# Kernel optimization log

Measured on AMD Instinct MI355X. Metric: run time of the kernel, lower is better.

The kernel has to match this reference:

```python
import jax, jax.numpy as jnp
import numpy as np

_SAMPLING_EPS = 1e-5
B, V = 256, 128000


def _apply_min_p(logits, min_p):
    # probs >= min_p * max_prob  <=>  keep; else logit -> -inf
    probs = jax.nn.softmax(logits, axis=-1)
    max_probs = jnp.max(probs, axis=-1, keepdims=True)
    keep = probs >= (min_p[:, None] * max_probs)
    return jnp.where(keep, logits, -jnp.inf)


def _apply_top_k_top_p(logits, top_k, top_p):
    # Sort ascending once; derive per-row keep-thresholds for both filters.
    logits_sort = jnp.sort(logits, axis=-1)  # [B, V] ascending
    # top-k threshold: value at position V-k (kth largest)
    k_idx = jnp.clip(V - top_k, 0, V - 1).astype(jnp.int32)
    k_thresh = jnp.take_along_axis(logits_sort, k_idx[:, None], axis=-1)  # [B,1]
    # top-p: on ascending-sorted probs, token is kept iff cumsum > 1 - p
    probs_sort = jax.nn.softmax(logits_sort, axis=-1)
    probs_cum = jnp.cumsum(probs_sort, axis=-1)
    kept = probs_cum > (1.0 - top_p[:, None])
    kept = kept.at[:, -1].set(True)  # always keep the max-prob token
    p_thresh = jnp.min(jnp.where(kept, logits_sort, jnp.inf), axis=-1, keepdims=True)
    thresh = jnp.maximum(k_thresh, p_thresh)
    return jnp.where(logits >= thresh, logits, -jnp.inf)


def setup_inputs() -> dict:
    key = jax.random.key(0)
    k1, k2, k3, k4, k5 = jax.random.split(key, 5)
    logits = jax.random.normal(k1, (B, V), jnp.float32)
    temperature = jax.random.uniform(k2, (B,), jnp.float32, 0.1, 1.5)
    temperature = temperature.at[:8].set(0.0)  # greedy rows
    min_p = jax.random.uniform(k3, (B,), jnp.float32, 0.0, 0.2)
    top_k = jax.random.randint(k4, (B,), 1, 64).astype(jnp.int32)
    top_p = jax.random.uniform(k5, (B,), jnp.float32, 0.5, 1.0)
    return {"logits": logits, "temperature": temperature, "min_p": min_p,
            "top_k": top_k, "top_p": top_p}


def reference(logits, temperature, min_p, top_k, top_p):
    logits = logits.astype(jnp.float32)
    greedy = jnp.argmax(logits, axis=-1)  # [B]
    # safe temperature divide (greedy rows have temp ~ 0 but are overridden)
    safe_t = jnp.where(temperature < _SAMPLING_EPS, 1.0, temperature)
    scaled = logits / safe_t[:, None]
    scaled = _apply_min_p(scaled, min_p)
    masked = _apply_top_k_top_p(scaled, top_k, top_p)
    # Gumbel-max trick == categorical sampling from softmax(masked)
    u = jax.random.uniform(jax.random.key(42), masked.shape, jnp.float32, 1e-10, 1.0)
    gumbel = -jnp.log(-jnp.log(u))
    random_sampled = jnp.argmax(masked + gumbel, axis=-1)
    sampled = jnp.where(temperature < _SAMPLING_EPS, greedy, random_sampled)
    return sampled[:, None]  # sampled_token_ids [B, 1]
```

## Files before the change

kernel.cpp:

```cpp
#include <hip/hip_runtime.h>
#include <hip/hip_cooperative_groups.h>
#include <stdint.h>

namespace cg = cooperative_groups;

typedef unsigned long long u64;
typedef unsigned int u32;

#define VOCAB 128000
#define NV4   32000
#define HV4   16000
#define NROWS 256
#define BLK   1024
#define NW    16
#define NB    4096
#define CAPL  2048
#define CAPLS 4096
#define SEPS  1e-5f
#define LN2X40 27.725887222397812f

#define WS_MASSH   0ull
#define WS_LIST    16777216ull
#define WS_CNTH    20971520ull
#define WS_PARTS   29360128ull
#define WS_PARTK   29362176ull
#define WS_PARTGV  29364224ull
#define WS_PARTGI  29366272ull
#define WS_LL      29368320ull
#define WS_KP      29369344ull
#define WS_NEED    29370368ull

__device__ __forceinline__ u32 f2key(float f){
  u32 u = __float_as_uint(f);
  return (u & 0x80000000u) ? ~u : (u | 0x80000000u);
}
__device__ __forceinline__ float key2f(u32 k){
  u32 u = (k & 0x80000000u) ? (k ^ 0x80000000u) : ~k;
  return __uint_as_float(u);
}

__device__ __forceinline__ void tf2x32(u32 x0, u32 x1, u32 &o0, u32 &o1){
  const u32 k0 = 0u, k1 = 42u, k2 = 0u ^ 42u ^ 0x1BD11BDAu;
  x0 += k0; x1 += k1;
#define TFR(r) { x0 += x1; x1 = (x1 << (r)) | (x1 >> (32 - (r))); x1 ^= x0; }
  TFR(13) TFR(15) TFR(26) TFR(6)
  x0 += k1; x1 += k2 + 1u;
  TFR(17) TFR(29) TFR(16) TFR(24)
  x0 += k2; x1 += k0 + 2u;
  TFR(13) TFR(15) TFR(26) TFR(6)
  x0 += k0; x1 += k1 + 3u;
  TFR(17) TFR(29) TFR(16) TFR(24)
  x0 += k1; x1 += k2 + 4u;
  TFR(13) TFR(15) TFR(26) TFR(6)
  x0 += k2; x1 += k0 + 5u;
#undef TFR
  o0 = x0; o1 = x1;
}
__device__ __forceinline__ u32 gumbel_bits(u32 i){
  u32 o0, o1; tf2x32(0u, i, o0, o1);
  return o0 ^ o1;
}
__device__ __forceinline__ float bits2gumbel(u32 b){
  float f = __uint_as_float(0x3F800000u | (b >> 9)) - 1.0f;
  float u = fmaxf(1e-10f, f + 1e-10f);
  return -logf(-logf(u));
}

__device__ __forceinline__ void cross4096_u32(
    const u32* arr, u32* aux, u32 target, u32* out_idx, u32* out_before, int t)
{
  aux[t] = arr[4*t+0] + arr[4*t+1] + arr[4*t+2] + arr[4*t+3];
  __syncthreads();
  if (t < 64){
    u32 gs = 0u;
    #pragma unroll
    for (int j=0;j<16;j++) gs += aux[t*16+j];
    u32 pref = gs;
    #pragma unroll
    for (int d=1; d<64; d<<=1){ u32 v = __shfl_up(pref, d, 64); if (t >= d) pref += v; }
    u64 bal = __ballot(pref > target);
    int g = bal ? (__ffsll((long long)bal) - 1) : 63;
    u32 pg = __shfl(pref, g, 64);
    u32 gg = __shfl(gs, g, 64);
    if (t == 0){
      u32 c = pg - gg;
      u32 idx = (u32)(g*64 + 63);
      for (int j=0;j<16;j++){
        u32 v = aux[g*16+j];
        if (c + v > target){
          int base = (g*16+j)*4;
          for (int q=0;q<4;q++){
            u32 w = arr[base+q];
            if (c + w > target){ idx = (u32)(base+q); goto doneu; }
            c += w;
          }
        }
        c += v;
      }
      doneu:
      *out_idx = idx; *out_before = c;
    }
  }
}

__device__ __forceinline__ void cross4096_u64(
    const u64* arr, u64* aux, u64 target, u32* out_idx, u64* out_before, int t)
{
  aux[t] = arr[4*t+0] + arr[4*t+1] + arr[4*t+2] + arr[4*t+3];
  __syncthreads();
  if (t < 64){
    u64 gs = 0ull;
    #pragma unroll
    for (int j=0;j<16;j++) gs += aux[t*16+j];
    u64 pref = gs;
    #pragma unroll
    for (int d=1; d<64; d<<=1){
      u64 v = __shfl_up((unsigned long long)pref, d, 64); if (t >= d) pref += v;
    }
    u64 bal = __ballot(pref > target);
    int g = bal ? (__ffsll((long long)bal) - 1) : 63;
    u64 pg = __shfl((unsigned long long)pref, g, 64);
    u64 gg = __shfl((unsigned long long)gs, g, 64);
    if (t == 0){
      u64 c = pg - gg;
      u32 idx = (u32)(g*64 + 63);
      for (int j=0;j<16;j++){
        u64 v = aux[g*16+j];
        if (c + v > target){
          int base = (g*16+j)*4;
          for (int q=0;q<4;q++){
            u64 w = arr[base+q];
            if (c + w > target){ idx = (u32)(base+q); goto donev; }
            c += w;
          }
        }
        c += v;
      }
      donev:
      *out_idx = idx; *out_before = c;
    }
  }
}

__device__ __forceinline__ void cross4096_mass(
    const u64* arr, u64* aux, float topp_v, u64* out_target,
    u32* out_idx, u64* out_before, int t)
{
  aux[t] = arr[4*t+0] + arr[4*t+1] + arr[4*t+2] + arr[4*t+3];
  __syncthreads();
  if (t < 64){
    u64 gs = 0ull;
    #pragma unroll
    for (int j=0;j<16;j++) gs += aux[t*16+j];
    u64 pref = gs;
    #pragma unroll
    for (int d=1; d<64; d<<=1){
      u64 v = __shfl_up((unsigned long long)pref, d, 64); if (t >= d) pref += v;
    }
    u64 total = __shfl((unsigned long long)pref, 63, 64);
    u64 target = (u64)((double)(1.0f - topp_v) * (double)total);
    u64 bal = __ballot(pref > target);
    int g = bal ? (__ffsll((long long)bal) - 1) : 63;
    u64 pg = __shfl((unsigned long long)pref, g, 64);
    u64 gg = __shfl((unsigned long long)gs, g, 64);
    if (t == 0){
      u64 c = pg - gg;
      u32 idx = (u32)(g*64 + 63);
      for (int j=0;j<16;j++){
        u64 v = aux[g*16+j];
        if (c + v > target){
          int base = (g*16+j)*4;
          for (int q=0;q<4;q++){
            u64 w = arr[base+q];
            if (c + w > target){ idx = (u32)(base+q); goto donem; }
            c += w;
          }
        }
        c += v;
      }
      donem:
      *out_target = target; *out_idx = idx; *out_before = c;
    }
  }
}

__device__ __forceinline__ void cross256_u32(const u32* arr, u32 target, u32* out_idx, int t){
  if (t < 64){
    u32 gs = arr[4*t+0]+arr[4*t+1]+arr[4*t+2]+arr[4*t+3];
    u32 pref = gs;
    #pragma unroll
    for (int d=1; d<64; d<<=1){ u32 v=__shfl_up(pref,d,64); if (t>=d) pref+=v; }
    u64 bal = __ballot(pref > target);
    int g = bal ? (__ffsll((long long)bal)-1) : 63;
    u32 pg=__shfl(pref,g,64), gg=__shfl(gs,g,64);
    if (t==0){
      u32 c = pg-gg; u32 idx=(u32)(g*4+3);
      for (int q=0;q<4;q++){ u32 w=arr[g*4+q]; if (c+w>target){ idx=(u32)(g*4+q); break; } c+=w; }
      *out_idx = idx;
    }
  }
}
__device__ __forceinline__ void cross256_u64(const u64* arr, u64 target, u32* out_idx, int t){
  if (t < 64){
    u64 gs = arr[4*t+0]+arr[4*t+1]+arr[4*t+2]+arr[4*t+3];
    u64 pref = gs;
    #pragma unroll
    for (int d=1; d<64; d<<=1){
      u64 v=__shfl_up((unsigned long long)pref,d,64); if (t>=d) pref+=v;
    }
    u64 bal = __ballot(pref > target);
    int g = bal ? (__ffsll((long long)bal)-1) : 63;
    u64 pg=__shfl((unsigned long long)pref,g,64), gg=__shfl((unsigned long long)gs,g,64);
    if (t==0){
      u64 c = pg-gg; u32 idx=(u32)(g*4+3);
      for (int q=0;q<4;q++){ u64 w=arr[g*4+q]; if (c+w>target){ idx=(u32)(g*4+q); break; } c+=w; }
      *out_idx = idx;
    }
  }
}

__device__ __forceinline__ void msmerge(float &m1, float &S1, float m2, float S2){
  float mm = fmaxf(m1, m2);
  if (mm == -INFINITY){ m1 = mm; S1 = 0.0f; return; }
  S1 = S1*__expf(m1-mm) + S2*__expf(m2-mm);
  m1 = mm;
}

__device__ __forceinline__ void argmax_write(
    float best, u32 bi, float* wrf, u32* wru, int ln, int wv, int b, int* out)
{
  #pragma unroll
  for (int d=32; d>0; d>>=1){
    float c2=__shfl_down(best,d,64); u32 i2=__shfl_down(bi,d,64);
    if (c2>best || (c2==best && i2<bi)){best=c2;bi=i2;}
  }
  if (ln==0){ wrf[wv]=best; wru[wv]=bi; }
  __syncthreads();
  if (wv==0){
    float b1=(ln<NW)?wrf[ln]:-INFINITY; u32 i1=(ln<NW)?wru[ln]:0xFFFFFFFFu;
    #pragma unroll
    for (int d=32; d>0; d>>=1){
      float b2=__shfl_down(b1,d,64); u32 i2=__shfl_down(i1,d,64);
      if (b2>b1 || (b2==b1 && i2<i1)){b1=b2;i1=i2;}
    }
    if (ln==0) out[b]=(int)i1;
  }
}

__global__ __launch_bounds__(BLK, 8) void k_coop(
    const float* __restrict__ logits, const float* __restrict__ temp,
    const float* __restrict__ minp, const int* __restrict__ topk,
    const float* __restrict__ topp, int* __restrict__ out, char* __restrict__ ws)
{
  cg::grid_group grid = cg::this_grid();

  __shared__ u32 cnt[NB];
  __shared__ u64 massI[NB];
  __shared__ u64 list[CAPL];
  __shared__ u64 aux64[BLK];
  __shared__ float wrf1[NW];
  __shared__ u32  wru1[NW], wru2[NW];
  __shared__ u32 sh_idx, sh_bef32, sh_lstar, sh_u1, sh_u2;
  __shared__ u64 sh_bef64, sh_tfix;

  u32* aux32 = (u32*)aux64;
  u64* massH  = (u64*)(ws + WS_MASSH);
  u64* wsList = (u64*)(ws + WS_LIST);
  u32* cntH   = (u32*)(ws + WS_CNTH);
  float* partS  = (float*)(ws + WS_PARTS);
  u32*   partK  = (u32*)(ws + WS_PARTK);
  float* partGV = (float*)(ws + WS_PARTGV);
  u32*   partGI = (u32*)(ws + WS_PARTGI);
  u32*   LL     = (u32*)(ws + WS_LL);
  u32*   KP     = (u32*)(ws + WS_KP);

  const int bid = blockIdx.x;
  const int r = bid >> 1;
  const int h = bid & 1;
  const int t = threadIdx.x;
  const int ln = t & 63, wv = t >> 6;
  const float T = temp[r];
  const bool greedy = (T < SEPS);
  const float invT = greedy ? 1.0f : (1.0f / T);
  const float* row = logits + (size_t)r * VOCAB;
  const float4* row4 = (const float4*)row;
  const int hb4 = h * HV4, he4 = hb4 + HV4;

  if (t == 0 && h == 0){ LL[r] = 0u; KP[r] = 0u; }
  if (greedy){
    float M = -INFINITY; u32 Mi = 0xFFFFFFFFu;
    for (int i = hb4 + t; i < he4; i += BLK){
      float4 q = row4[i];
      #pragma unroll
      for (int j=0;j<4;j++){
        float l = (&q.x)[j]; u32 gi = (u32)(i*4+j);
        if (l > M){ M = l; Mi = gi; }
      }
    }
    #pragma unroll
    for (int d=32; d>0; d>>=1){
      float M2=__shfl_down(M,d,64); u32 I2=__shfl_down(Mi,d,64);
      if (M2>M || (M2==M && I2<Mi)){ M=M2; Mi=I2; }
    }
    if (ln==0){ wrf1[wv]=M; wru1[wv]=Mi; }
    __syncthreads();
    if (t==0){
      float b1=wrf1[0]; u32 i1=wru1[0];
      for (int w=1; w<NW; w++){
        if (wrf1[w]>b1 || (wrf1[w]==b1 && wru1[w]<i1)){ b1=wrf1[w]; i1=wru1[w]; }
      }
      partGV[bid]=b1; partGI[bid]=i1;
    }
  } else {
    for (int i=t;i<NB;i+=BLK) cnt[i]=0u;
    __syncthreads();
    u32 km = 0u;
    float S0=0.0f,S1=0.0f,S2=0.0f,S3=0.0f;
#define PA(LV, SS) { \
    float l_=(LV); u32 k_=f2key(l_); \
    if (k_>km) km=k_; \
    atomicAdd(&cnt[k_>>20], 1u); \
    SS += __expf(l_*invT); }
    for (int i = hb4 + t; i < he4; i += 2*BLK){
      float4 qa = row4[i];
      int i2 = i + BLK; bool h2 = (i2 < he4);
      float4 qb; if (h2) qb = row4[i2];
      PA(qa.x,S0) PA(qa.y,S1) PA(qa.z,S2) PA(qa.w,S3)
      if (h2){ PA(qb.x,S0) PA(qb.y,S1) PA(qb.z,S2) PA(qb.w,S3) }
    }
#undef PA
    float S = (S0+S1)+(S2+S3);
    #pragma unroll
    for (int d=32; d>0; d>>=1){
      S += __shfl_down(S,d,64);
      u32 k2 = __shfl_down(km,d,64); if (k2>km) km=k2;
    }
    if (ln==0){ wrf1[wv]=S; wru1[wv]=km; }
    __syncthreads();
    for (int i=t;i<NB;i+=BLK) cntH[(size_t)bid*NB + i] = cnt[i];
    if (t==0){
      float St=0.0f; u32 kt=0u;
      for (int w=0; w<NW; w++){ St += wrf1[w]; if (wru1[w]>kt) kt=wru1[w]; }
      partS[bid]=St; partK[bid]=kt;
    }
  }
  __threadfence();
  grid.sync();

  float m=0.0f, Z=1.0f, cs=0.0f;
  u32 b1k=0u, r1=1u, lstar=0u, CLB=0u;
  int tk=1; bool kcert=false, fastOK=false;

  if (greedy){
    if (h==0 && t==0){
      float vA=partGV[bid], vB=partGV[bid+1];
      u32 iA=partGI[bid], iB=partGI[bid+1];
      out[r] = (vB>vA || (vB==vA && iB<iA)) ? (int)iB : (int)iA;
    }
  } else {
    const int pb = bid ^ 1;
    for (int i=t;i<NB;i+=BLK) cnt[i] += cntH[(size_t)pb*NB + i];
    {
      u32 kA = partK[bid & ~1], kB = partK[bid | 1];
      float SA = partS[bid & ~1], SB = partS[bid | 1];
      u32 kmax = kA > kB ? kA : kB;
      m = key2f(kmax) * invT;
      Z = (SA + SB) * __expf(-m);
    }
    cs = LN2X40 - m;
    __syncthreads();

    tk = topk[r]; if (tk < 1) tk = 1; if (tk > VOCAB) tk = VOCAB;
    cross4096_u32(cnt, aux32, (u32)(VOCAB - tk), &sh_idx, &sh_bef32, t);
    __syncthreads();
    b1k = sh_idx;
    r1  = (u32)(VOCAB - tk + 1) - sh_bef32;

    if (wv==0){
      const float rhs = minp[r] * (1.0f / Z);
      u32 lo = 0u, hi = 0xFF800000u;
      while (hi - lo > 64u){
        u32 step = (hi - lo) >> 6;
        u32 k = lo + (u32)(ln + 1) * step;
        float e = __expf(fmaf(key2f(k), invT, -m));
        u64 bal = __ballot((e / Z) >= rhs);
        if (bal){
          u32 g = (u32)(__ffsll((long long)bal) - 1);
          hi = lo + (g + 1u) * step;
          lo = lo + g * step;
        } else {
          lo += 64u * step;
        }
      }
      u32 k = lo + 1u + (u32)ln;
      bool ok = (k <= hi);
      float e = __expf(fmaf(key2f(k), invT, -m));
      u64 bal = __ballot(ok && ((e / Z) >= rhs));
      if (ln==0) sh_lstar = bal ? (lo + 1u + (u32)(__ffsll((long long)bal) - 1)) : hi;
    }
    __syncthreads();
    lstar = sh_lstar;
    const u32 bl = lstar >> 20;

    {
      u32 pa=0u, pc=0u;
      for (int i=t;i<NB;i+=BLK){
        u32 c = cnt[i];
        if ((u32)i > bl)   pa += c;
        if ((u32)i >= b1k) pc += c;
      }
      #pragma unroll
      for (int d=32; d>0; d>>=1){ pa += __shfl_down(pa,d,64); pc += __shfl_down(pc,d,64); }
      if (ln==0){ wru1[wv]=pa; wru2[wv]=pc; }
      __syncthreads();
      if (t==0){
        u32 a=0u, c2=0u;
        for (int w=0; w<NW; w++){ a += wru1[w]; c2 += wru2[w]; }
        sh_u1 = a; sh_u2 = c2;
      }
      __syncthreads();
    }
    const u32 Kmin = sh_u1;
    kcert = (Kmin >= (u32)tk);
    CLB = kcert ? b1k : bl;
    const u32 listCnt = kcert ? sh_u2 : (Kmin + cnt[bl]);
    fastOK = (listCnt <= (u32)CAPL);
  }

  if (!greedy){
    for (int i=t;i<NB;i+=BLK) massI[i]=0ull;
    __syncthreads();
    u32 kc = 0u;
#define PC(LV, IDX) { \
    float l_ = (LV); u32 key_ = f2key(l_); \
    if (key_ >= lstar){ \
      kc++; \
      u64 lm_ = (u64)__expf(fmaf(l_, invT, cs)); \
      if (lm_) atomicAdd(&massI[key_>>20], lm_); \
    } \
    bool cand_ = fastOK && ((key_>>20) >= CLB); \
    u64 bal_ = __ballot(cand_); \
    if (cand_){ \
      u32 lead_ = (u32)__ffsll((long long)bal_) - 1u; \
      u32 base_ = 0u; \
      if ((u32)ln == lead_) base_ = atomicAdd(&LL[r], (u32)__popcll(bal_)); \
      base_ = __shfl(base_, (int)lead_, 64); \
      u32 p_ = base_ + (u32)__popcll(bal_ & ((1ull << ln) - 1ull)); \
      if (p_ < CAPL) wsList[(size_t)r*CAPL + p_] = ((u64)key_ << 32) | (u64)(u32)(IDX); \
    } }
    for (int i = hb4 + t; i < he4; i += 2*BLK){
      float4 qa = row4[i];
      int i2 = i + BLK; bool h2 = (i2 < he4);
      float4 qb; if (h2) qb = row4[i2];
      PC(qa.x,i*4+0) PC(qa.y,i*4+1) PC(qa.z,i*4+2) PC(qa.w,i*4+3)
      if (h2){ PC(qb.x,i2*4+0) PC(qb.y,i2*4+1) PC(qb.z,i2*4+2) PC(qb.w,i2*4+3) }
    }
#undef PC
    #pragma unroll
    for (int d=32; d>0; d>>=1) kc += __shfl_down(kc, d, 64);
    if (ln==0) wru1[wv] = kc;
    __syncthreads();
    if (t==0){
      u32 K2=0u; for (int w=0;w<NW;w++) K2 += wru1[w];
      atomicAdd(&KP[r], K2);
    }
    if (h==1){
      for (int i=t;i<NB;i+=BLK) massH[(size_t)bid*NB + i] = massI[i];
    }
  }
  __threadfence();
  grid.sync();

  if (greedy || h != 0) return;

  for (int i=t;i<NB;i+=BLK) massI[i] += massH[(size_t)(bid+1)*NB + i];
  __syncthreads();
  const u32 K = KP[r];
  const bool kval = (K >= (u32)tk);
  u32 llen = LL[r]; if (llen > (u32)CAPL) llen = CAPL;

  cross4096_mass(massI, aux64, topp[r], &sh_tfix, &sh_idx, &sh_bef64, t);
  __syncthreads();
  const u32 b1p = sh_idx;
  const u64 t1  = sh_tfix - sh_bef64;
  const bool needK = kval && (b1p <= b1k);
  const bool needP = (!kval) || (b1p >= b1k);

  u32 kkey = 0u, pkey = 0u;

  if (fastOK){
    for (u32 i=t; i<llen; i+=BLK) list[i] = wsList[(size_t)r*CAPL + i];
    __syncthreads();
    if (needK){
      for (int i=t;i<NB;i+=BLK) cnt[i]=0u;
      __syncthreads();
      for (u32 i=t; i<llen; i+=BLK){
        u32 key = (u32)(list[i]>>32);
        if ((key>>20) == b1k) atomicAdd(&cnt[(key>>8)&0xFFFu], 1u);
      }
      __syncthreads();
      cross4096_u32(cnt, aux32, r1-1u, &sh_idx, &sh_bef32, t);
      __syncthreads();
      u32 b2k = sh_idx, r2 = r1 - sh_bef32;
      u32 prefk = (b1k<<12) | b2k;
      for (int i=t;i<256;i+=BLK) cnt[i]=0u;
      __syncthreads();
      for (u32 i=t; i<llen; i+=BLK){
        u32 key = (u32)(list[i]>>32);
        if ((key>>8) == prefk) atomicAdd(&cnt[key&0xFFu], 1u);
      }
      __syncthreads();
      cross256_u32(cnt, r2-1u, &sh_idx, t);
      __syncthreads();
      kkey = (prefk<<8) | sh_idx;
    }
    if (needP){
      for (int i=t;i<NB;i+=BLK) massI[i]=0ull;
      __syncthreads();
      for (u32 i=t; i<llen; i+=BLK){
        u32 key = (u32)(list[i]>>32);
        if ((key>>20) == b1p && key >= lstar){
          u64 lm = (u64)__expf(fmaf(key2f(key), invT, cs));
          if (lm) atomicAdd(&massI[(key>>8)&0xFFFu], lm);
        }
      }
      __syncthreads();
      cross4096_u64(massI, aux64, t1, &sh_idx, &sh_bef64, t);
      __syncthreads();
      u32 b2p = sh_idx; u64 t2 = t1 - sh_bef64;
      u32 prefp = (b1p<<12) | b2p;
      for (int i=t;i<256;i+=BLK) massI[i]=0ull;
      __syncthreads();
      for (u32 i=t; i<llen; i+=BLK){
        u32 key = (u32)(list[i]>>32);
        if ((key>>8) == prefp && key >= lstar){
          u64 lm = (u64)__expf(fmaf(key2f(key), invT, cs));
          if (lm) atomicAdd(&massI[key&0xFFu], lm);
        }
      }
      __syncthreads();
      cross256_u64(massI, t2, &sh_idx, t);
      __syncthreads();
      pkey = (prefp<<8) | sh_idx;
    }
    const u32 thrkey = kkey > pkey ? kkey : pkey;

    float best = -INFINITY; u32 bi = 0xFFFFFFFFu;
    for (u32 i=t; i<llen; i+=BLK){
      u64 e = list[i];
      u32 key = (u32)(e>>32);
      if (key >= thrkey){
        u32 idx = (u32)e;
        u32 c = (u32)r * (u32)VOCAB + idx;
        float cand = key2f(key)*invT + bits2gumbel(gumbel_bits(c));
        if (cand > best || (cand == best && idx < bi)){ best = cand; bi = idx; }
      }
    }
    argmax_write(best, bi, wrf1, wru1, ln, wv, r, out);
    return;
  }

  for (int i=t;i<NB;i+=BLK) cnt[i]=0u;
  { __syncthreads(); }
  for (int i=t;i<NB;i+=BLK) massI[i]=0ull;
  __syncthreads();
  for (int i=t; i<NV4; i+=BLK){
    float4 q = row4[i];
    #pragma unroll
    for (int j=0;j<4;j++){
      float l = (&q.x)[j]; u32 key = f2key(l); u32 hb = key>>20;
      if (needK && hb == b1k) atomicAdd(&cnt[(key>>8)&0xFFFu], 1u);
      if (needP && hb == b1p && key >= lstar){
        u64 lm = (u64)__expf(fmaf(l, invT, cs));
        if (lm) atomicAdd(&massI[(key>>8)&0xFFFu], lm);
      }
    }
  }
  __syncthreads();
  u32 b2k = 0u, r2 = 1u, b2p = 0u; u64 t2 = 0ull;
  if (needK){
    cross4096_u32(cnt, aux32, r1-1u, &sh_idx, &sh_bef32, t);
    __syncthreads();
    b2k = sh_idx; r2 = r1 - sh_bef32;
  }
  if (needP){
    cross4096_u64(massI, aux64, t1, &sh_idx, &sh_bef64, t);
    __syncthreads();
    b2p = sh_idx; t2 = t1 - sh_bef64;
  }
  const u32 prefk = (b1k<<12) | b2k;
  const u32 prefp = (b1p<<12) | b2p;
  for (int i=t;i<256;i+=BLK){ cnt[i]=0u; massI[i]=0ull; }
  __syncthreads();
  for (int i=t; i<NV4; i+=BLK){
    float4 q = row4[i];
    #pragma unroll
    for (int j=0;j<4;j++){
      float l = (&q.x)[j]; u32 key = f2key(l);
      if (needK && (key>>8) == prefk) atomicAdd(&cnt[key&0xFFu], 1u);
      if (needP && (key>>8) == prefp && key >= lstar){
        u64 lm = (u64)__expf(fmaf(l, invT, cs));
        if (lm) atomicAdd(&massI[key&0xFFu], lm);
      }
    }
  }
  __syncthreads();
  if (needK){
    cross256_u32(cnt, r2-1u, &sh_idx, t);
    __syncthreads();
    kkey = (prefk<<8) | sh_idx;
  }
  if (needP){
    cross256_u64(massI, t2, &sh_idx, t);
    __syncthreads();
    pkey = (prefp<<8) | sh_idx;
  }
  const float thrf = key2f(kkey > pkey ? kkey : pkey);
  float best = -INFINITY; u32 bi = 0xFFFFFFFFu;
  for (int i=t; i<NV4; i+=BLK){
    float4 q = row4[i];
    #pragma unroll
    for (int j=0;j<4;j++){
      float l = (&q.x)[j];
      if (l >= thrf){
        u32 idx = (u32)(i*4+j);
        u32 c = (u32)r * (u32)VOCAB + idx;
        float cand = l*invT + bits2gumbel(gumbel_bits(c));
        if (cand > best || (cand == best && idx < bi)){ best = cand; bi = idx; }
      }
    }
  }
  argmax_write(best, bi, wrf1, wru1, ln, wv, r, out);
}

__global__ __launch_bounds__(BLK) void k_single(
    const float* __restrict__ logits, const float* __restrict__ temp,
    const float* __restrict__ minp, const int* __restrict__ topk,
    const float* __restrict__ topp, int* __restrict__ out)
{
  __shared__ u32 cnt[NB];
  __shared__ u64 massI[NB];
  __shared__ u64 list[CAPLS];
  __shared__ u64 aux64[BLK];
  __shared__ float wrf1[NW], wrf2[NW];
  __shared__ u32  wru1[NW], wru2[NW];
  __shared__ float sh_m, sh_Z;
  __shared__ u32 sh_lstar, sh_len, sh_idx, sh_bef32, sh_u1, sh_u2, sh_u3;
  __shared__ u64 sh_bef64, sh_tfix;

  u32* aux32 = (u32*)aux64;

  const int b = blockIdx.x;
  const int t = threadIdx.x;
  const int ln = t & 63, wv = t >> 6;
  const float T = temp[b];
  const float* row = logits + (size_t)b * VOCAB;
  const float4* row4 = (const float4*)row;

  if (T < SEPS){
    float M = -INFINITY; u32 Mi = 0xFFFFFFFFu;
    for (int i=t; i<NV4; i+=BLK){
      float4 q = row4[i];
      #pragma unroll
      for (int j=0;j<4;j++){
        float l = (&q.x)[j]; u32 gi = (u32)(i*4+j);
        if (l > M){ M = l; Mi = gi; }
      }
    }
    argmax_write(M, Mi, wrf1, wru1, ln, wv, b, out);
    return;
  }

  const float invT = 1.0f / T;
  for (int i=t;i<NB;i+=BLK){ cnt[i]=0u; massI[i]=0ull; }
  if (t==0) sh_len=0u;
  __syncthreads();

  float ms0=-INFINITY,S0=0.0f, ms1=-INFINITY,S1=0.0f,
        ms2=-INFINITY,S2=0.0f, ms3=-INFINITY,S3=0.0f;
#define ONLINE(LV, MS, SS) { \
    float l_ = (LV); \
    atomicAdd(&cnt[f2key(l_)>>20], 1u); \
    float s_ = l_ * invT; \
    float d_ = s_ - MS; \
    float e_ = __expf(-fabsf(d_)); \
    if (d_ > 0.0f){ SS = fmaf(SS, e_, 1.0f); MS = s_; } else { SS += e_; } \
  }
  for (int i=t; i<NV4; i+=2*BLK){
    float4 qa = row4[i];
    int i2 = i + BLK; bool h2 = (i2 < NV4);
    float4 qb; if (h2) qb = row4[i2];
    ONLINE(qa.x,ms0,S0) ONLINE(qa.y,ms1,S1) ONLINE(qa.z,ms2,S2) ONLINE(qa.w,ms3,S3)
    if (h2){
      ONLINE(qb.x,ms0,S0) ONLINE(qb.y,ms1,S1) ONLINE(qb.z,ms2,S2) ONLINE(qb.w,ms3,S3)
    }
  }
#undef ONLINE
  msmerge(ms0,S0,ms1,S1); msmerge(ms2,S2,ms3,S3); msmerge(ms0,S0,ms2,S2);
  #pragma unroll
  for (int d=32; d>0; d>>=1){
    float mz = __shfl_down(ms0, d, 64); float Sz = __shfl_down(S0, d, 64);
    msmerge(ms0, S0, mz, Sz);
  }
  if (ln==0){ wrf1[wv]=ms0; wrf2[wv]=S0; }
  __syncthreads();
  if (wv==0){
    float m1 = (ln<NW)? wrf1[ln] : -INFINITY;
    float Sx = (ln<NW)? wrf2[ln] : 0.0f;
    #pragma unroll
    for (int d=32; d>0; d>>=1){
      float mz=__shfl_down(m1,d,64); float Sz=__shfl_down(Sx,d,64);
      msmerge(m1, Sx, mz, Sz);
    }
    if (ln==0){ sh_m = m1; sh_Z = Sx; }
  }
  __syncthreads();
  const float m = sh_m, Z = sh_Z;

  int tk = topk[b]; if (tk < 1) tk = 1; if (tk > VOCAB) tk = VOCAB;
  cross4096_u32(cnt, aux32, (u32)(VOCAB - tk), &sh_idx, &sh_bef32, t);
  __syncthreads();
  const u32 b1k = sh_idx;
  const u32 r1  = (u32)(VOCAB - tk + 1) - sh_bef32;

  if (wv==0){
    const float rhs = minp[b] * (1.0f / Z);
    u32 lo = 0u, hi = 0xFF800000u;
    while (hi - lo > 64u){
      u32 step = (hi - lo) >> 6;
      u32 k = lo + (u32)(ln + 1) * step;
      float e = __expf(fmaf(key2f(k), invT, -m));
      u64 bal = __ballot((e / Z) >= rhs);
      if (bal){
        u32 g = (u32)(__ffsll((long long)bal) - 1);
        hi = lo + (g + 1u) * step;
        lo = lo + g * step;
      } else {
        lo += 64u * step;
      }
    }
    u32 k = lo + 1u + (u32)ln;
    bool ok = (k <= hi);
    float e = __expf(fmaf(key2f(k), invT, -m));
    u64 bal = __ballot(ok && ((e / Z) >= rhs));
    if (ln==0) sh_lstar = bal ? (lo + 1u + (u32)(__ffsll((long long)bal) - 1)) : hi;
  }
  __syncthreads();
  const u32 lstar = sh_lstar;
  const u32 bl = lstar >> 20;

  {
    u32 pa=0u, pc=0u;
    for (int i=t;i<NB;i+=BLK){
      u32 c = cnt[i];
      if ((u32)i > bl)   pa += c;
      if ((u32)i >= b1k) pc += c;
    }
    #pragma unroll
    for (int d=32; d>0; d>>=1){ pa += __shfl_down(pa,d,64); pc += __shfl_down(pc,d,64); }
    if (ln==0){ wru1[wv]=pa; wru2[wv]=pc; }
    __syncthreads();
    if (t==0){
      u32 a=0u, c2=0u;
      for (int w=0; w<NW; w++){ a += wru1[w]; c2 += wru2[w]; }
      sh_u1 = a; sh_u2 = c2;
    }
    __syncthreads();
  }
  const u32 Kmin = sh_u1;
  const bool kcert = (Kmin >= (u32)tk);
  const u32 CLB = kcert ? b1k : bl;
  const u32 listlen = kcert ? sh_u2 : (Kmin + cnt[bl]);
  const bool fastOK = (listlen <= (u32)CAPLS);
  const float cs = LN2X40 - m;

  u32 kc = 0u;
#define P2E(LV, IDX) { \
    float l_ = (LV); u32 key_ = f2key(l_); \
    if (key_ >= lstar){ \
      kc++; \
      u64 lm_ = (u64)__expf(fmaf(l_, invT, cs)); \
      if (lm_) atomicAdd(&massI[key_>>20], lm_); \
    } \
    if (fastOK && (key_>>20) >= CLB){ \
      u32 p_ = atomicAdd(&sh_len, 1u); \
      if (p_ < CAPLS) list[p_] = ((u64)key_ << 32) | (u64)(u32)(IDX); \
    } \
  }
  for (int i=t; i<NV4; i+=2*BLK){
    float4 qa = row4[i];
    int i2 = i + BLK; bool h2 = (i2 < NV4);
    float4 qb; if (h2) qb = row4[i2];
    P2E(qa.x, i*4+0) P2E(qa.y, i*4+1) P2E(qa.z, i*4+2) P2E(qa.w, i*4+3)
    if (h2){
      P2E(qb.x, i2*4+0) P2E(qb.y, i2*4+1) P2E(qb.z, i2*4+2) P2E(qb.w, i2*4+3)
    }
  }
#undef P2E
  #pragma unroll
  for (int d=32; d>0; d>>=1) kc += __shfl_down(kc, d, 64);
  if (ln==0) wru1[wv] = kc;
  __syncthreads();
  if (t==0){ u32 K2=0u; for (int w=0;w<NW;w++) K2 += wru1[w]; sh_u3 = K2; }
  __syncthreads();
  const u32 K = sh_u3;
  const bool kval = (K >= (u32)tk);
  const u32 llen = sh_len;

  cross4096_mass(massI, aux64, topp[b], &sh_tfix, &sh_idx, &sh_bef64, t);
  __syncthreads();
  const u32 b1p = sh_idx;
  const u64 t1  = sh_tfix - sh_bef64;
  const bool needK = kval && (b1p <= b1k);
  const bool needP = (!kval) || (b1p >= b1k);

  u32 kkey = 0u, pkey = 0u;

  if (fastOK){
    if (needK){
      for (int i=t;i<NB;i+=BLK) cnt[i]=0u;
      __syncthreads();
      for (u32 i=t; i<llen; i+=BLK){
        u32 key = (u32)(list[i]>>32);
        if ((key>>20) == b1k) atomicAdd(&cnt[(key>>8)&0xFFFu], 1u);
      }
      __syncthreads();
      cross4096_u32(cnt, aux32, r1-1u, &sh_idx, &sh_bef32, t);
      __syncthreads();
      u32 b2k = sh_idx, r2 = r1 - sh_bef32;
      u32 prefk = (b1k<<12) | b2k;
      for (int i=t;i<256;i+=BLK) cnt[i]=0u;
      __syncthreads();
      for (u32 i=t; i<llen; i+=BLK){
        u32 key = (u32)(list[i]>>32);
        if ((key>>8) == prefk) atomicAdd(&cnt[key&0xFFu], 1u);
      }
      __syncthreads();
      cross256_u32(cnt, r2-1u, &sh_idx, t);
      __syncthreads();
      kkey = (prefk<<8) | sh_idx;
    }
    if (needP){
      for (int i=t;i<NB;i+=BLK) massI[i]=0ull;
      __syncthreads();
      for (u32 i=t; i<llen; i+=BLK){
        u32 key = (u32)(list[i]>>32);
        if ((key>>20) == b1p && key >= lstar){
          u64 lm = (u64)__expf(fmaf(key2f(key), invT, cs));
          if (lm) atomicAdd(&massI[(key>>8)&0xFFFu], lm);
        }
      }
      __syncthreads();
      cross4096_u64(massI, aux64, t1, &sh_idx, &sh_bef64, t);
      __syncthreads();
      u32 b2p = sh_idx; u64 t2 = t1 - sh_bef64;
      u32 prefp = (b1p<<12) | b2p;
      for (int i=t;i<256;i+=BLK) massI[i]=0ull;
      __syncthreads();
      for (u32 i=t; i<llen; i+=BLK){
        u32 key = (u32)(list[i]>>32);
        if ((key>>8) == prefp && key >= lstar){
          u64 lm = (u64)__expf(fmaf(key2f(key), invT, cs));
          if (lm) atomicAdd(&massI[key&0xFFu], lm);
        }
      }
      __syncthreads();
      cross256_u64(massI, t2, &sh_idx, t);
      __syncthreads();
      pkey = (prefp<<8) | sh_idx;
    }
    const u32 thrkey = kkey > pkey ? kkey : pkey;

    float best = -INFINITY; u32 bi = 0xFFFFFFFFu;
    for (u32 i=t; i<llen; i+=BLK){
      u64 e = list[i];
      u32 key = (u32)(e>>32);
      if (key >= thrkey){
        u32 idx = (u32)e;
        u32 c = (u32)b * (u32)VOCAB + idx;
        float cand = key2f(key)*invT + bits2gumbel(gumbel_bits(c));
        if (cand > best || (cand == best && idx < bi)){ best = cand; bi = idx; }
      }
    }
    argmax_write(best, bi, wrf1, wru1, ln, wv, b, out);
    return;
  }

  for (int i=t;i<NB;i+=BLK){ cnt[i]=0u; massI[i]=0ull; }
  __syncthreads();
  for (int i=t; i<NV4; i+=BLK){
    float4 q = row4[i];
    #pragma unroll
    for (int j=0;j<4;j++){
      float l = (&q.x)[j]; u32 key = f2key(l); u32 hb = key>>20;
      if (needK && hb == b1k) atomicAdd(&cnt[(key>>8)&0xFFFu], 1u);
      if (needP && hb == b1p && key >= lstar){
        u64 lm = (u64)__expf(fmaf(l, invT, cs));
        if (lm) atomicAdd(&massI[(key>>8)&0xFFFu], lm);
      }
    }
  }
  __syncthreads();
  u32 b2k = 0u, r2 = 1u, b2p = 0u; u64 t2 = 0ull;
  if (needK){
    cross4096_u32(cnt, aux32, r1-1u, &sh_idx, &sh_bef32, t);
    __syncthreads();
    b2k = sh_idx; r2 = r1 - sh_bef32;
  }
  if (needP){
    cross4096_u64(massI, aux64, t1, &sh_idx, &sh_bef64, t);
    __syncthreads();
    b2p = sh_idx; t2 = t1 - sh_bef64;
  }
  const u32 prefk = (b1k<<12) | b2k;
  const u32 prefp = (b1p<<12) | b2p;
  for (int i=t;i<256;i+=BLK){ cnt[i]=0u; massI[i]=0ull; }
  __syncthreads();
  for (int i=t; i<NV4; i+=BLK){
    float4 q = row4[i];
    #pragma unroll
    for (int j=0;j<4;j++){
      float l = (&q.x)[j]; u32 key = f2key(l);
      if (needK && (key>>8) == prefk) atomicAdd(&cnt[key&0xFFu], 1u);
      if (needP && (key>>8) == prefp && key >= lstar){
        u64 lm = (u64)__expf(fmaf(l, invT, cs));
        if (lm) atomicAdd(&massI[key&0xFFu], lm);
      }
    }
  }
  __syncthreads();
  if (needK){
    cross256_u32(cnt, r2-1u, &sh_idx, t);
    __syncthreads();
    kkey = (prefk<<8) | sh_idx;
  }
  if (needP){
    cross256_u64(massI, t2, &sh_idx, t);
    __syncthreads();
    pkey = (prefp<<8) | sh_idx;
  }
  const float thrf = key2f(kkey > pkey ? kkey : pkey);
  float best = -INFINITY; u32 bi = 0xFFFFFFFFu;
  for (int i=t; i<NV4; i+=BLK){
    float4 q = row4[i];
    #pragma unroll
    for (int j=0;j<4;j++){
      float l = (&q.x)[j];
      if (l >= thrf){
        u32 idx = (u32)(i*4+j);
        u32 c = (u32)b * (u32)VOCAB + idx;
        float cand = l*invT + bits2gumbel(gumbel_bits(c));
        if (cand > best || (cand == best && idx < bi)){ best = cand; bi = idx; }
      }
    }
  }
  argmax_write(best, bi, wrf1, wru1, ln, wv, b, out);
}

extern "C" void kernel_launch(void* const* d_in, const int* in_sizes, int n_in,
                              void* d_out, int out_size, void* d_ws, size_t ws_size,
                              hipStream_t stream)
{
  const float* logits = (const float*)d_in[0];
  const float* temp   = (const float*)d_in[1];
  const float* minp   = (const float*)d_in[2];
  const int*   topk   = (const int*)d_in[3];
  const float* topp   = (const float*)d_in[4];
  int* out = (int*)d_out;
  char* ws = (char*)d_ws;

  int maxb = 0;
  hipError_t oe = hipOccupancyMaxActiveBlocksPerMultiprocessor(&maxb, k_coop, BLK, 0);
  const bool coop_ok = (ws_size >= (size_t)WS_NEED) && (oe == hipSuccess) && (maxb >= 2);

  if (coop_ok){
    void* args[] = { (void*)&logits, (void*)&temp, (void*)&minp, (void*)&topk,
                     (void*)&topp, (void*)&out, (void*)&ws };
    hipLaunchCooperativeKernel(k_coop, dim3(2*NROWS), dim3(BLK), args, 0, stream);
  } else {
    hipLaunchKernelGGL(k_single, dim3(NROWS), dim3(BLK), 0, stream,
                       logits, temp, minp, topk, topp, out);
  }
}
```

Baseline: 59.40 us.

## Replace grid-wide syncs with pairwise flag handshakes between row-half blocks

Swaps the two cooperative grid.sync barriers for per-pair flag signalling in global memory, so each block waits only for its partner block handling the other half of the same row. Greedy rows exit early, and the second-half block exits after publishing its mass histogram. This is meant to remove the cost of grid-wide barriers and the stalls caused by the slowest rows. In exchange it adds a memset launch to clear the flags and relies on spin-waits on flags, which assume both blocks of a pair are co-resident.

Measured after the change: 59.21 us. About the same (-0.3%).

```diff
diff --git a/kernel.cpp b/kernel.cpp
--- a/kernel.cpp
+++ b/kernel.cpp
@@ -1,8 +1,5 @@
 #include <hip/hip_runtime.h>
-#include <hip/hip_cooperative_groups.h>
 #include <stdint.h>
-
-namespace cg = cooperative_groups;
 
 typedef unsigned long long u64;
 typedef unsigned int u32;
@@ -28,7 +25,9 @@
 #define WS_PARTGI  29366272ull
 #define WS_LL      29368320ull
 #define WS_KP      29369344ull
-#define WS_NEED    29370368ull
+#define WS_FLAGA   29370368ull
+#define WS_FLAGC   29372416ull
+#define WS_NEED    29374464ull
 
 __device__ __forceinline__ u32 f2key(float f){
   u32 u = __float_as_uint(f);
@@ -252,8 +251,6 @@
     const float* __restrict__ minp, const int* __restrict__ topk,
     const float* __restrict__ topp, int* __restrict__ out, char* __restrict__ ws)
 {
-  cg::grid_group grid = cg::this_grid();
-
   __shared__ u32 cnt[NB];
   __shared__ u64 massI[NB];
   __shared__ u64 list[CAPL];
@@ -273,6 +270,8 @@
   u32*   partGI = (u32*)(ws + WS_PARTGI);
   u32*   LL     = (u32*)(ws + WS_LL);
   u32*   KP     = (u32*)(ws + WS_KP);
+  u32*   flagA  = (u32*)(ws + WS_FLAGA);
+  u32*   flagC  = (u32*)(ws + WS_FLAGC);
 
   const int bid = blockIdx.x;
   const int r = bid >> 1;
@@ -286,7 +285,8 @@
   const float4* row4 = (const float4*)row;
   const int hb4 = h * HV4, he4 = hb4 + HV4;
 
-  if (t == 0 && h == 0){ LL[r] = 0u; KP[r] = 0u; }
+  if (t == 0 && h == 0){ atomicExch(&LL[r], 0u); atomicExch(&KP[r], 0u); }
+
   if (greedy){
     float M = -INFINITY; u32 Mi = 0xFFFFFFFFu;
     for (int i = hb4 + t; i < he4; i += BLK){
@@ -310,10 +310,22 @@
         if (wrf1[w]>b1 || (wrf1[w]==b1 && wru1[w]<i1)){ b1=wrf1[w]; i1=wru1[w]; }
       }
       partGV[bid]=b1; partGI[bid]=i1;
-    }
-  } else {
-    for (int i=t;i<NB;i+=BLK) cnt[i]=0u;
-    __syncthreads();
+      __threadfence();
+      atomicExch(&flagA[bid], 1u);
+      if (h==0){
+        while (atomicAdd(&flagA[bid^1], 0u) == 0u) __builtin_amdgcn_s_sleep(2);
+        __threadfence();
+        float vA=partGV[bid], vB=partGV[bid^1];
+        u32 iA=partGI[bid], iB=partGI[bid^1];
+        out[r] = (vB>vA || (vB==vA && iB<iA)) ? (int)iB : (int)iA;
+      }
+    }
+    return;
+  }
+
+  for (int i=t;i<NB;i+=BLK) cnt[i]=0u;
+  __syncthreads();
+  {
     u32 km = 0u;
     float S0=0.0f,S1=0.0f,S2=0.0f,S3=0.0f;
 #define PA(LV, SS) { \
@@ -344,20 +356,20 @@
       partS[bid]=St; partK[bid]=kt;
     }
   }
-  __threadfence();
-  grid.sync();
+  __syncthreads();
+  if (t==0){
+    __threadfence();
+    atomicExch(&flagA[bid], 1u);
+    while (atomicAdd(&flagA[bid^1], 0u) == 0u) __builtin_amdgcn_s_sleep(2);
+    __threadfence();
+  }
+  __syncthreads();
 
   float m=0.0f, Z=1.0f, cs=0.0f;
   u32 b1k=0u, r1=1u, lstar=0u, CLB=0u;
   int tk=1; bool kcert=false, fastOK=false;
 
-  if (greedy){
-    if (h==0 && t==0){
-      float vA=partGV[bid], vB=partGV[bid+1];
-      u32 iA=partGI[bid], iB=partGI[bid+1];
-      out[r] = (vB>vA || (vB==vA && iB<iA)) ? (int)iB : (int)iA;
-    }
-  } else {
+  {
     const int pb = bid ^ 1;
     for (int i=t;i<NB;i+=BLK) cnt[i] += cntH[(size_t)pb*NB + i];
     {
@@ -427,7 +439,7 @@
     fastOK = (listCnt <= (u32)CAPL);
   }
 
-  if (!greedy){
+  {
     for (int i=t;i<NB;i+=BLK) massI[i]=0ull;
     __syncthreads();
     u32 kc = 0u;
@@ -464,20 +476,27 @@
       u32 K2=0u; for (int w=0;w<NW;w++) K2 += wru1[w];
       atomicAdd(&KP[r], K2);
     }
-    if (h==1){
-      for (int i=t;i<NB;i+=BLK) massH[(size_t)bid*NB + i] = massI[i];
-    }
-  }
-  __threadfence();
-  grid.sync();
-
-  if (greedy || h != 0) return;
+  }
+  if (h==1){
+    for (int i=t;i<NB;i+=BLK) massH[(size_t)bid*NB + i] = massI[i];
+    __syncthreads();
+    if (t==0){ __threadfence(); atomicExch(&flagC[bid], 1u); }
+    return;
+  }
+  __syncthreads();
+  if (t==0){
+    while (atomicAdd(&flagC[bid^1], 0u) == 0u) __builtin_amdgcn_s_sleep(2);
+    __threadfence();
+    sh_u1 = atomicAdd(&KP[r], 0u);
+    sh_u2 = atomicAdd(&LL[r], 0u);
+  }
+  __syncthreads();
 
   for (int i=t;i<NB;i+=BLK) massI[i] += massH[(size_t)(bid+1)*NB + i];
-  __syncthreads();
-  const u32 K = KP[r];
+  const u32 K = sh_u1;
   const bool kval = (K >= (u32)tk);
-  u32 llen = LL[r]; if (llen > (u32)CAPL) llen = CAPL;
+  u32 llen = sh_u2; if (llen > (u32)CAPL) llen = CAPL;
+  __syncthreads();
 
   cross4096_mass(massI, aux64, topp[r], &sh_tfix, &sh_idx, &sh_bef64, t);
   __syncthreads();
@@ -561,7 +580,7 @@
   }
 
   for (int i=t;i<NB;i+=BLK) cnt[i]=0u;
-  { __syncthreads(); }
+  __syncthreads();
   for (int i=t;i<NB;i+=BLK) massI[i]=0ull;
   __syncthreads();
   for (int i=t; i<NV4; i+=BLK){
@@ -974,6 +993,7 @@
   const bool coop_ok = (ws_size >= (size_t)WS_NEED) && (oe == hipSuccess) && (maxb >= 2);
 
   if (coop_ok){
+    hipMemsetAsync(ws + WS_FLAGA, 0, 4096, stream);
     void* args[] = { (void*)&logits, (void*)&temp, (void*)&minp, (void*)&topk,
                      (void*)&topp, (void*)&out, (void*)&ws };
     hipLaunchCooperativeKernel(k_coop, dim3(2*NROWS), dim3(BLK), args, 0, stream);
```
